# Kernel optimization log

Hardware: AMD Instinct MI355X
Metric: run time of the kernel (lower is better)

The kernel has to match this reference:

```python
import jax, jax.numpy as jnp
import numpy as np

C_IN = 3072
C_OUT = 1024
MAJ = 3  # majority_size


def setup_inputs() -> dict:
    key = jax.random.key(0)
    k1, k2 = jax.random.split(key)
    x = jax.random.normal(k1, (256, C_IN), dtype=jnp.float32)
    stdv = 1.0 / np.sqrt(C_OUT * C_IN)
    weight = jax.random.uniform(k2, (C_OUT, C_IN), dtype=jnp.float32, minval=-stdv, maxval=stdv)
    return {"input": x, "weight": weight}


def reference(input, weight):
    B = input.shape[0]
    G = C_IN // MAJ  # number of majority groups
    # Deterministic binarization (sign), as in Binarize(..., 'det')
    xb = jnp.sign(input)            # [B, C_IN]
    wb = jnp.sign(weight)           # [C_OUT, C_IN]
    # Grouped products: inter[b,c,g] = sum_k xb[b,g,k] * wb[c,g,k]
    # (equivalent to einsum('bj,cj->bcj') followed by reshape+sum over groups of 3)
    xg = xb.reshape(B, G, MAJ)
    wg = wb.reshape(C_OUT, G, MAJ)
    inter = jnp.einsum('bgk,cgk->bcg', xg, wg)  # [B, C_OUT, G]
    # Majority vote: clamp group sums to [-1, 1], sum across groups, scale by 2.25
    out = jnp.sum(jnp.clip(inter, -1.0, 1.0), axis=2) * 2.25  # [B, C_OUT]
    return out
```

## Files before the change

kernel.cpp:

```cpp
#include <hip/hip_runtime.h>
#include <stdint.h>


#define C_IN  3072
#define C_OUT 1024
#define BT 32
#define CT 32
#define PSTR 49

__global__ __launch_bounds__(1024) void majfc_one(const float* __restrict__ x,
                                                  const float* __restrict__ w,
                                                  float* __restrict__ out) {
    __shared__ uint64_t xp[BT][PSTR];
    __shared__ uint64_t wp[CT][PSTR];

    const int tid  = threadIdx.x;
    const int lane = tid & 63;
    const int wv   = tid >> 6;

    const int r  = blockIdx.x & 7;
    const int s  = blockIdx.x >> 3;
    const int ct = r * 4 + (s & 3);
    const int bt = s >> 2;
    const int b0 = bt * BT;
    const int c0 = ct * CT;

#pragma unroll 4
    for (int i = 0; i < 16; ++i) {
        const int q    = i >> 2;
        const int rowc = (i & 3) * 16 + wv;
        const float* src = ((rowc < 32) ? (x + (size_t)(b0 + rowc) * C_IN)
                                        : (w + (size_t)(c0 + rowc - 32) * C_IN))
                           + q * 768 + 12 * lane;
        const float4* s4 = (const float4*)src;
        float4 f0 = s4[0], f1 = s4[1], f2 = s4[2];
        uint64_t pl0  = __ballot(f0.x > 0.0f);
        uint64_t pl1  = __ballot(f0.y > 0.0f);
        uint64_t pl2  = __ballot(f0.z > 0.0f);
        uint64_t pl3  = __ballot(f0.w > 0.0f);
        uint64_t pl4  = __ballot(f1.x > 0.0f);
        uint64_t pl5  = __ballot(f1.y > 0.0f);
        uint64_t pl6  = __ballot(f1.z > 0.0f);
        uint64_t pl7  = __ballot(f1.w > 0.0f);
        uint64_t pl8  = __ballot(f2.x > 0.0f);
        uint64_t pl9  = __ballot(f2.y > 0.0f);
        uint64_t pl10 = __ballot(f2.z > 0.0f);
        uint64_t pl11 = __ballot(f2.w > 0.0f);
        if (lane == 0) {
            uint64_t* d = (rowc < 32) ? &xp[rowc][q * 12] : &wp[rowc - 32][q * 12];
            d[0] = pl0;  d[1] = pl1;  d[2]  = pl2;  d[3]  = pl3;
            d[4] = pl4;  d[5] = pl5;  d[6]  = pl6;  d[7]  = pl7;
            d[8] = pl8;  d[9] = pl9;  d[10] = pl10; d[11] = pl11;
        }
    }
    __syncthreads();

    const int cl = tid & 31;
    const int bl = tid >> 5;
    int acc = 0;
#pragma unroll
    for (int q = 0; q < 4; ++q) {
        uint64_t X[12], W[12];
#pragma unroll
        for (int m = 0; m < 12; ++m) {
            X[m] = xp[bl][q * 12 + m];
            W[m] = wp[cl][q * 12 + m];
        }
#pragma unroll
        for (int j = 0; j < 4; ++j) {
            uint64_t t0 = X[3 * j + 0] ^ W[3 * j + 0];
            uint64_t t1 = X[3 * j + 1] ^ W[3 * j + 1];
            uint64_t t2 = X[3 * j + 2] ^ W[3 * j + 2];
            acc += __popcll((t0 & t1) | (t2 & (t0 | t1)));
        }
    }
    out[(size_t)(b0 + bl) * C_OUT + c0 + cl] = 2304.0f - 4.5f * (float)acc;
}

extern "C" void kernel_launch(void* const* d_in, const int* in_sizes, int n_in,
                              void* d_out, int out_size, void* d_ws, size_t ws_size,
                              hipStream_t stream) {
    const float* x = (const float*)d_in[0];
    const float* w = (const float*)d_in[1];
    float* out = (float*)d_out;
    (void)d_ws; (void)ws_size;

    majfc_one<<<256, 1024, 0, stream>>>(x, w, out);
}
```

Before: 76.34 us.

## Pack sign bits once globally with cooperative grid sync, then tile from workspace

Before, each block re-read and binarized its own 32 x-rows and 32 w-rows, so every input row was packed by many blocks (x 32 times, w 8 times). Now the whole grid first packs each row once into a global workspace of bit-planes, synchronizes across the grid, and then each block loads its packed tiles into LDS. This removes the redundant float reads and ballots. In exchange it adds a grid-wide barrier, a cooperative launch, and a round trip of the packed data through global memory.

New measurement: 109.0 us. +42.7%, slower.

```diff
diff --git a/kernel.cpp b/kernel.cpp
--- a/kernel.cpp
+++ b/kernel.cpp
@@ -1,6 +1,9 @@
 #include <hip/hip_runtime.h>
+#include <hip/hip_cooperative_groups.h>
 #include <stdint.h>
 
+
+namespace cg = cooperative_groups;
 
 #define C_IN  3072
 #define C_OUT 1024
@@ -8,15 +11,53 @@
 #define CT 32
 #define PSTR 49
 
-__global__ __launch_bounds__(1024) void majfc_one(const float* __restrict__ x,
-                                                  const float* __restrict__ w,
-                                                  float* __restrict__ out) {
+
+__device__ __forceinline__ void pack_job(int j, const float* __restrict__ x,
+                                         const float* __restrict__ w,
+                                         uint64_t* __restrict__ pk, int lane) {
+    const int row = j >> 2;
+    const int q   = j & 3;
+    const float* src = ((row < 256) ? (x + (size_t)row * C_IN)
+                                    : (w + (size_t)(row - 256) * C_IN))
+                       + q * 768 + 12 * lane;
+    const float4* s4 = (const float4*)src;
+    float4 f0 = s4[0], f1 = s4[1], f2 = s4[2];
+    uint64_t pl0  = __ballot(f0.x > 0.0f);
+    uint64_t pl1  = __ballot(f0.y > 0.0f);
+    uint64_t pl2  = __ballot(f0.z > 0.0f);
+    uint64_t pl3  = __ballot(f0.w > 0.0f);
+    uint64_t pl4  = __ballot(f1.x > 0.0f);
+    uint64_t pl5  = __ballot(f1.y > 0.0f);
+    uint64_t pl6  = __ballot(f1.z > 0.0f);
+    uint64_t pl7  = __ballot(f1.w > 0.0f);
+    uint64_t pl8  = __ballot(f2.x > 0.0f);
+    uint64_t pl9  = __ballot(f2.y > 0.0f);
+    uint64_t pl10 = __ballot(f2.z > 0.0f);
+    uint64_t pl11 = __ballot(f2.w > 0.0f);
+    if (lane == 0) {
+        uint64_t* d = pk + (size_t)row * 48 + q * 12;
+        d[0] = pl0;  d[1] = pl1;  d[2]  = pl2;  d[3]  = pl3;
+        d[4] = pl4;  d[5] = pl5;  d[6]  = pl6;  d[7]  = pl7;
+        d[8] = pl8;  d[9] = pl9;  d[10] = pl10; d[11] = pl11;
+    }
+}
+
+__global__ __launch_bounds__(1024) void majfc_coop(const float* __restrict__ x,
+                                                   const float* __restrict__ w,
+                                                   uint64_t* __restrict__ pk,
+                                                   float* __restrict__ out) {
     __shared__ uint64_t xp[BT][PSTR];
     __shared__ uint64_t wp[CT][PSTR];
 
     const int tid  = threadIdx.x;
     const int lane = tid & 63;
     const int wv   = tid >> 6;
+    const int W    = blockIdx.x * 16 + wv;
+
+    pack_job(W, x, w, pk, lane);
+    if (W < 1024) pack_job(W + 4096, x, w, pk, lane);
+
+    cg::this_grid().sync();
 
     const int r  = blockIdx.x & 7;
     const int s  = blockIdx.x >> 3;
@@ -25,33 +66,13 @@
     const int b0 = bt * BT;
     const int c0 = ct * CT;
 
-#pragma unroll 4
-    for (int i = 0; i < 16; ++i) {
-        const int q    = i >> 2;
-        const int rowc = (i & 3) * 16 + wv;
-        const float* src = ((rowc < 32) ? (x + (size_t)(b0 + rowc) * C_IN)
-                                        : (w + (size_t)(c0 + rowc - 32) * C_IN))
-                           + q * 768 + 12 * lane;
-        const float4* s4 = (const float4*)src;
-        float4 f0 = s4[0], f1 = s4[1], f2 = s4[2];
-        uint64_t pl0  = __ballot(f0.x > 0.0f);
-        uint64_t pl1  = __ballot(f0.y > 0.0f);
-        uint64_t pl2  = __ballot(f0.z > 0.0f);
-        uint64_t pl3  = __ballot(f0.w > 0.0f);
-        uint64_t pl4  = __ballot(f1.x > 0.0f);
-        uint64_t pl5  = __ballot(f1.y > 0.0f);
-        uint64_t pl6  = __ballot(f1.z > 0.0f);
-        uint64_t pl7  = __ballot(f1.w > 0.0f);
-        uint64_t pl8  = __ballot(f2.x > 0.0f);
-        uint64_t pl9  = __ballot(f2.y > 0.0f);
-        uint64_t pl10 = __ballot(f2.z > 0.0f);
-        uint64_t pl11 = __ballot(f2.w > 0.0f);
-        if (lane == 0) {
-            uint64_t* d = (rowc < 32) ? &xp[rowc][q * 12] : &wp[rowc - 32][q * 12];
-            d[0] = pl0;  d[1] = pl1;  d[2]  = pl2;  d[3]  = pl3;
-            d[4] = pl4;  d[5] = pl5;  d[6]  = pl6;  d[7]  = pl7;
-            d[8] = pl8;  d[9] = pl9;  d[10] = pl10; d[11] = pl11;
-        }
+#pragma unroll
+    for (int i = 0; i < 3; ++i) {
+        const int p   = tid + i * 1024;
+        const int row = p / 48;
+        const int m   = p - row * 48;
+        if (row < 32) xp[row][m]      = pk[(size_t)(b0 + row) * 48 + m];
+        else          wp[row - 32][m] = pk[(size_t)(256 + c0 + row - 32) * 48 + m];
     }
     __syncthreads();
 
@@ -60,17 +81,17 @@
     int acc = 0;
 #pragma unroll
     for (int q = 0; q < 4; ++q) {
-        uint64_t X[12], W[12];
+        uint64_t X[12], Wr[12];
 #pragma unroll
         for (int m = 0; m < 12; ++m) {
-            X[m] = xp[bl][q * 12 + m];
-            W[m] = wp[cl][q * 12 + m];
+            X[m]  = xp[bl][q * 12 + m];
+            Wr[m] = wp[cl][q * 12 + m];
         }
 #pragma unroll
         for (int j = 0; j < 4; ++j) {
-            uint64_t t0 = X[3 * j + 0] ^ W[3 * j + 0];
-            uint64_t t1 = X[3 * j + 1] ^ W[3 * j + 1];
-            uint64_t t2 = X[3 * j + 2] ^ W[3 * j + 2];
+            uint64_t t0 = X[3 * j + 0] ^ Wr[3 * j + 0];
+            uint64_t t1 = X[3 * j + 1] ^ Wr[3 * j + 1];
+            uint64_t t2 = X[3 * j + 2] ^ Wr[3 * j + 2];
             acc += __popcll((t0 & t1) | (t2 & (t0 | t1)));
         }
     }
@@ -83,7 +104,9 @@
     const float* x = (const float*)d_in[0];
     const float* w = (const float*)d_in[1];
     float* out = (float*)d_out;
-    (void)d_ws; (void)ws_size;
+    uint64_t* pk = (uint64_t*)d_ws;
 
-    majfc_one<<<256, 1024, 0, stream>>>(x, w, out);
+    void* args[] = {(void*)&x, (void*)&w, (void*)&pk, (void*)&out};
+    hipLaunchCooperativeKernel((void*)majfc_coop, dim3(256), dim3(1024),
+                               args, 0, stream);
 }
```
